# Kernel optimization log

Hardware: AMD Instinct MI355X
Metric: run time of the kernel (lower is better)

## Reference

```python
import jax, jax.numpy as jnp
import numpy as np

N, IN, OUT = 4096, 256, 256


def setup_inputs() -> dict:
    key = jax.random.key(0)
    k = jax.random.split(key, 7)
    return {
        "x": jax.random.normal(k[0], (N, IN), dtype=jnp.float32),
        "eps_w": jax.random.normal(k[1], (N, IN, OUT), dtype=jnp.float32),
        "eps_b": jax.random.normal(k[2], (N, OUT), dtype=jnp.float32),
        # learned parameters (init ranges per the torch module)
        "w_param1": jax.random.uniform(k[3], (IN, OUT), minval=-0.01, maxval=0.01, dtype=jnp.float32),
        "logw_param2": jax.random.uniform(k[4], (IN, OUT), minval=-4.0, maxval=-2.0, dtype=jnp.float32),
        "b_param1": jax.random.uniform(k[5], (OUT,), minval=-0.01, maxval=0.01, dtype=jnp.float32),
        "logb_param2": jax.random.uniform(k[6], (OUT,), minval=-4.0, maxval=-2.0, dtype=jnp.float32),
    }


def reference(x, eps_w, eps_b, w_param1, logw_param2, b_param1, logb_param2):
    # Per-sample reparameterized Gaussian weights: Normal(mu, exp(log_sigma)).sample((N,))
    weights = w_param1[None] + jnp.exp(logw_param2)[None] * eps_w   # [N, IN, OUT]
    biases = b_param1[None] + jnp.exp(logb_param2)[None] * eps_b    # [N, OUT]
    # (x.unsqueeze(1) @ weights).squeeze(1) + biases  ->  batched matvec
    return jnp.einsum("ni,nio->no", x, weights) + biases
```

## Files before the change

kernel.cpp:

```cpp
#include <hip/hip_runtime.h>

#define N_ROWS  4096
#define IN_DIM  256
#define OUT_DIM 256

#define RA 4
#define TA 256

#define RB 8
#define TB 512
#define TI 32
#define NTILES (IN_DIM / TI)

typedef float f32x4 __attribute__((ext_vector_type(4)));

__device__ __forceinline__ float4 nt_load4(const float4* p) {
    f32x4 v = __builtin_nontemporal_load((const f32x4*)p);
    return make_float4(v.x, v.y, v.z, v.w);
}

__global__ void bayes_exp_kernel(const float* __restrict__ logw,
                                 const float* __restrict__ logb,
                                 float* __restrict__ sw,
                                 float* __restrict__ sb) {
    int idx = blockIdx.x * blockDim.x + threadIdx.x;
    if (idx < IN_DIM * OUT_DIM) sw[idx] = __expf(logw[idx]);
    if (idx < OUT_DIM)          sb[idx] = __expf(logb[idx]);
}

template <bool PRE>
__global__ __launch_bounds__(TA) void bayes_base_kernel(
    const float* __restrict__ x,
    const float* __restrict__ eps_b,
    const float* __restrict__ w1,
    const float* __restrict__ b1,
    const float* __restrict__ sbl,
    float* __restrict__ out)
{
    __shared__ float xs[RA * IN_DIM];
    const int tid = threadIdx.x;
    const int n0  = blockIdx.x * RA;

    ((float4*)xs)[tid] = ((const float4*)(x + (size_t)n0 * IN_DIM))[tid];
    __syncthreads();

    const int row = tid >> 6;
    const int o4  = tid & 63;
    const int n   = n0 + row;

    const float4* w4 = (const float4*)w1 + o4;
    float4 acc = make_float4(0.f, 0.f, 0.f, 0.f);

    #pragma unroll 4
    for (int i = 0; i < IN_DIM; ++i) {
        const float  xv = xs[row * IN_DIM + i];
        const float4 w  = w4[i * (OUT_DIM / 4)];
        acc.x = fmaf(xv, w.x, acc.x);
        acc.y = fmaf(xv, w.y, acc.y);
        acc.z = fmaf(xv, w.z, acc.z);
        acc.w = fmaf(xv, w.w, acc.w);
    }

    const float4 eb = nt_load4((const float4*)(eps_b + (size_t)n * OUT_DIM) + o4);
    const float4 b  = ((const float4*)b1)[o4];
    float4 sb       = ((const float4*)sbl)[o4];
    if (!PRE) {
        sb.x = __expf(sb.x); sb.y = __expf(sb.y);
        sb.z = __expf(sb.z); sb.w = __expf(sb.w);
    }

    float4 res;
    res.x = acc.x + fmaf(sb.x, eb.x, b.x);
    res.y = acc.y + fmaf(sb.y, eb.y, b.y);
    res.z = acc.z + fmaf(sb.z, eb.z, b.z);
    res.w = acc.w + fmaf(sb.w, eb.w, b.w);

    ((float4*)(out + (size_t)n * OUT_DIM))[o4] = res;
}

template <bool PRE>
__global__ __launch_bounds__(TB) void bayes_eps_kernel(
    const float* __restrict__ x,
    const float* __restrict__ eps_w,
    const float* __restrict__ swl,
    float* __restrict__ out)
{
    __shared__ float xs[RB * IN_DIM];
    __shared__ float st[2 * TI * OUT_DIM];

    const int tid = threadIdx.x;
    const int n0  = blockIdx.x * RB;

    ((float4*)xs)[tid] = ((const float4*)(x + (size_t)n0 * IN_DIM))[tid];

    const int row = tid >> 6;
    const int o4  = tid & 63;
    const int n   = n0 + row;

    const float4* e4base = (const float4*)(eps_w + (size_t)n * IN_DIM * OUT_DIM) + o4;

    const float4 base = ((const float4*)(out + (size_t)n * OUT_DIM))[o4];

    #define STAGE(t, b)                                                        \
        do {                                                                   \
            const float4* _src = (const float4*)(swl + (t) * TI * OUT_DIM);    \
            float4 _v[4];                                                      \
            _Pragma("unroll")                                                  \
            for (int _k = 0; _k < 4; ++_k) _v[_k] = _src[tid + _k * TB];       \
            if (!PRE) {                                                        \
                _Pragma("unroll")                                              \
                for (int _k = 0; _k < 4; ++_k) {                               \
                    _v[_k].x = __expf(_v[_k].x); _v[_k].y = __expf(_v[_k].y);  \
                    _v[_k].z = __expf(_v[_k].z); _v[_k].w = __expf(_v[_k].w);  \
                }                                                              \
            }                                                                  \
            float4* _dst = (float4*)(st + (b) * TI * OUT_DIM);                 \
            _Pragma("unroll")                                                  \
            for (int _k = 0; _k < 4; ++_k) _dst[tid + _k * TB] = _v[_k];       \
        } while (0)

    STAGE(0, 0);

    float4 acc = make_float4(0.f, 0.f, 0.f, 0.f);
    int cur = 0;

    for (int t = 0; t < NTILES; ++t) {
        __syncthreads();
        if (t + 1 < NTILES) STAGE(t + 1, cur ^ 1);

        const float4* e4 = e4base + (size_t)t * TI * (OUT_DIM / 4);
        const float4* sp = (const float4*)(st + cur * TI * OUT_DIM);

        #pragma unroll 4
        for (int i = 0; i < TI; ++i) {
            const float  xv = xs[row * IN_DIM + t * TI + i];
            const float4 s  = sp[i * 64 + o4];
            const float4 e  = nt_load4(e4 + i * 64);
            acc.x = fmaf(xv * s.x, e.x, acc.x);
            acc.y = fmaf(xv * s.y, e.y, acc.y);
            acc.z = fmaf(xv * s.z, e.z, acc.z);
            acc.w = fmaf(xv * s.w, e.w, acc.w);
        }
        cur ^= 1;
    }
    #undef STAGE

    float4 res;
    res.x = base.x + acc.x;
    res.y = base.y + acc.y;
    res.z = base.z + acc.z;
    res.w = base.w + acc.w;
    ((float4*)(out + (size_t)n * OUT_DIM))[o4] = res;
}

extern "C" void kernel_launch(void* const* d_in, const int* in_sizes, int n_in,
                              void* d_out, int out_size, void* d_ws, size_t ws_size,
                              hipStream_t stream) {
    const float* x     = (const float*)d_in[0];
    const float* eps_w = (const float*)d_in[1];
    const float* eps_b = (const float*)d_in[2];
    const float* w1    = (const float*)d_in[3];
    const float* logw2 = (const float*)d_in[4];
    const float* b1    = (const float*)d_in[5];
    const float* logb2 = (const float*)d_in[6];
    float* out = (float*)d_out;

    const size_t need = (size_t)(IN_DIM * OUT_DIM + OUT_DIM) * sizeof(float);

    if (ws_size >= need) {
        float* sw = (float*)d_ws;
        float* sb = sw + IN_DIM * OUT_DIM;
        bayes_exp_kernel<<<(IN_DIM * OUT_DIM + 255) / 256, 256, 0, stream>>>(
            logw2, logb2, sw, sb);
        bayes_base_kernel<true><<<N_ROWS / RA, TA, 0, stream>>>(
            x, eps_b, w1, b1, sb, out);
        bayes_eps_kernel<true><<<N_ROWS / RB, TB, 0, stream>>>(
            x, eps_w, sw, out);
    } else {
        bayes_base_kernel<false><<<N_ROWS / RA, TA, 0, stream>>>(
            x, eps_b, w1, b1, logb2, out);
        bayes_eps_kernel<false><<<N_ROWS / RB, TB, 0, stream>>>(
            x, eps_w, logw2, out);
    }
}
```

Baseline: 209.1 us.

## Hold full bf16 sigma matrix in LDS and widen blocks to 1024 threads

The exponentiated sigma weights are now precomputed as bf16 and loaded whole into shared memory (128 KB) once per block. This replaces the double-buffered fp32 tile staging and its per-tile barriers. Blocks grow to 1024 threads covering 16 rows, and the bias exp moves into the base kernel so that kernel runs independently of the workspace. bf16 sigma loses precision, and the large LDS footprint allows only one block per CU, which may limit latency hiding for the eps_w stream that dominates the cost.

```diff
diff --git a/kernel.cpp b/kernel.cpp
--- a/kernel.cpp
+++ b/kernel.cpp
@@ -4,13 +4,10 @@
 #define IN_DIM  256
 #define OUT_DIM 256
 
-#define RA 4
-#define TA 256
-
-#define RB 8
-#define TB 512
-#define TI 32
-#define NTILES (IN_DIM / TI)
+#define TA 1024
+#define RA 16
+#define TB 1024
+#define RB 16
 
 typedef float f32x4 __attribute__((ext_vector_type(4)));
 
@@ -19,22 +16,27 @@
     return make_float4(v.x, v.y, v.z, v.w);
 }
 
-__global__ void bayes_exp_kernel(const float* __restrict__ logw,
-                                 const float* __restrict__ logb,
-                                 float* __restrict__ sw,
-                                 float* __restrict__ sb) {
-    int idx = blockIdx.x * blockDim.x + threadIdx.x;
-    if (idx < IN_DIM * OUT_DIM) sw[idx] = __expf(logw[idx]);
-    if (idx < OUT_DIM)          sb[idx] = __expf(logb[idx]);
+__device__ __forceinline__ unsigned short f32_to_bf16(float f) {
+    unsigned u = __float_as_uint(f);
+    u += 0x7FFFu + ((u >> 16) & 1u);
+    return (unsigned short)(u >> 16);
+}
+__device__ __forceinline__ float bf16_to_f32(unsigned short h) {
+    return __uint_as_float(((unsigned)h) << 16);
 }
 
-template <bool PRE>
+__global__ void bayes_exp_kernel(const float* __restrict__ logw,
+                                 unsigned short* __restrict__ swb) {
+    int idx = blockIdx.x * blockDim.x + threadIdx.x;
+    if (idx < IN_DIM * OUT_DIM) swb[idx] = f32_to_bf16(__expf(logw[idx]));
+}
+
 __global__ __launch_bounds__(TA) void bayes_base_kernel(
     const float* __restrict__ x,
     const float* __restrict__ eps_b,
     const float* __restrict__ w1,
     const float* __restrict__ b1,
-    const float* __restrict__ sbl,
+    const float* __restrict__ logb2,
     float* __restrict__ out)
 {
     __shared__ float xs[RA * IN_DIM];
@@ -63,17 +65,13 @@
 
     const float4 eb = nt_load4((const float4*)(eps_b + (size_t)n * OUT_DIM) + o4);
     const float4 b  = ((const float4*)b1)[o4];
-    float4 sb       = ((const float4*)sbl)[o4];
-    if (!PRE) {
-        sb.x = __expf(sb.x); sb.y = __expf(sb.y);
-        sb.z = __expf(sb.z); sb.w = __expf(sb.w);
-    }
+    const float4 lb = ((const float4*)logb2)[o4];
 
     float4 res;
-    res.x = acc.x + fmaf(sb.x, eb.x, b.x);
-    res.y = acc.y + fmaf(sb.y, eb.y, b.y);
-    res.z = acc.z + fmaf(sb.z, eb.z, b.z);
-    res.w = acc.w + fmaf(sb.w, eb.w, b.w);
+    res.x = acc.x + fmaf(__expf(lb.x), eb.x, b.x);
+    res.y = acc.y + fmaf(__expf(lb.y), eb.y, b.y);
+    res.z = acc.z + fmaf(__expf(lb.z), eb.z, b.z);
+    res.w = acc.w + fmaf(__expf(lb.w), eb.w, b.w);
 
     ((float4*)(out + (size_t)n * OUT_DIM))[o4] = res;
 }
@@ -82,75 +80,65 @@
 __global__ __launch_bounds__(TB) void bayes_eps_kernel(
     const float* __restrict__ x,
     const float* __restrict__ eps_w,
-    const float* __restrict__ swl,
+    const void*  __restrict__ swsrc,
     float* __restrict__ out)
 {
+    __shared__ uint4 swbuf[IN_DIM * OUT_DIM / 8];
     __shared__ float xs[RB * IN_DIM];
-    __shared__ float st[2 * TI * OUT_DIM];
 
     const int tid = threadIdx.x;
     const int n0  = blockIdx.x * RB;
 
+    if (PRE) {
+        const uint4* src = (const uint4*)swsrc;
+        #pragma unroll
+        for (int r = 0; r < 8; ++r)
+            swbuf[tid + r * TB] = src[tid + r * TB];
+    } else {
+        const float4* src = (const float4*)swsrc;
+        unsigned short* dst = (unsigned short*)swbuf;
+        #pragma unroll
+        for (int r = 0; r < 16; ++r) {
+            const int   j = tid + r * TB;
+            const float4 v = src[j];
+            ushort4 h;
+            h.x = f32_to_bf16(__expf(v.x));
+            h.y = f32_to_bf16(__expf(v.y));
+            h.z = f32_to_bf16(__expf(v.z));
+            h.w = f32_to_bf16(__expf(v.w));
+            *(ushort4*)(dst + j * 4) = h;
+        }
+    }
     ((float4*)xs)[tid] = ((const float4*)(x + (size_t)n0 * IN_DIM))[tid];
+    __syncthreads();
 
     const int row = tid >> 6;
     const int o4  = tid & 63;
     const int n   = n0 + row;
 
-    const float4* e4base = (const float4*)(eps_w + (size_t)n * IN_DIM * OUT_DIM) + o4;
-
-    const float4 base = ((const float4*)(out + (size_t)n * OUT_DIM))[o4];
-
-    #define STAGE(t, b)                                                        \
-        do {                                                                   \
-            const float4* _src = (const float4*)(swl + (t) * TI * OUT_DIM);    \
-            float4 _v[4];                                                      \
-            _Pragma("unroll")                                                  \
-            for (int _k = 0; _k < 4; ++_k) _v[_k] = _src[tid + _k * TB];       \
-            if (!PRE) {                                                        \
-                _Pragma("unroll")                                              \
-                for (int _k = 0; _k < 4; ++_k) {                               \
-                    _v[_k].x = __expf(_v[_k].x); _v[_k].y = __expf(_v[_k].y);  \
-                    _v[_k].z = __expf(_v[_k].z); _v[_k].w = __expf(_v[_k].w);  \
-                }                                                              \
-            }                                                                  \
-            float4* _dst = (float4*)(st + (b) * TI * OUT_DIM);                 \
-            _Pragma("unroll")                                                  \
-            for (int _k = 0; _k < 4; ++_k) _dst[tid + _k * TB] = _v[_k];       \
-        } while (0)
-
-    STAGE(0, 0);
+    const unsigned short* swp = (const unsigned short*)swbuf;
+    const float4* e4 = (const float4*)(eps_w + (size_t)n * IN_DIM * OUT_DIM) + o4;
 
     float4 acc = make_float4(0.f, 0.f, 0.f, 0.f);
-    int cur = 0;
 
-    for (int t = 0; t < NTILES; ++t) {
-        __syncthreads();
-        if (t + 1 < NTILES) STAGE(t + 1, cur ^ 1);
+    #pragma unroll 8
+    for (int i = 0; i < IN_DIM; ++i) {
+        const float   xv = xs[row * IN_DIM + i];
+        const ushort4 h  = *(const ushort4*)(swp + i * OUT_DIM + o4 * 4);
+        const float4  e  = nt_load4(e4 + i * (OUT_DIM / 4));
+        acc.x = fmaf(xv * bf16_to_f32(h.x), e.x, acc.x);
+        acc.y = fmaf(xv * bf16_to_f32(h.y), e.y, acc.y);
+        acc.z = fmaf(xv * bf16_to_f32(h.z), e.z, acc.z);
+        acc.w = fmaf(xv * bf16_to_f32(h.w), e.w, acc.w);
+    }
 
-        const float4* e4 = e4base + (size_t)t * TI * (OUT_DIM / 4);
-        const float4* sp = (const float4*)(st + cur * TI * OUT_DIM);
-
-        #pragma unroll 4
-        for (int i = 0; i < TI; ++i) {
-            const float  xv = xs[row * IN_DIM + t * TI + i];
-            const float4 s  = sp[i * 64 + o4];
-            const float4 e  = nt_load4(e4 + i * 64);
-            acc.x = fmaf(xv * s.x, e.x, acc.x);
-            acc.y = fmaf(xv * s.y, e.y, acc.y);
-            acc.z = fmaf(xv * s.z, e.z, acc.z);
-            acc.w = fmaf(xv * s.w, e.w, acc.w);
-        }
-        cur ^= 1;
-    }
-    #undef STAGE
-
-    float4 res;
-    res.x = base.x + acc.x;
-    res.y = base.y + acc.y;
-    res.z = base.z + acc.z;
-    res.w = base.w + acc.w;
-    ((float4*)(out + (size_t)n * OUT_DIM))[o4] = res;
+    float4* op = (float4*)(out + (size_t)n * OUT_DIM) + o4;
+    float4 base = *op;
+    base.x += acc.x;
+    base.y += acc.y;
+    base.z += acc.z;
+    base.w += acc.w;
+    *op = base;
 }
 
 extern "C" void kernel_launch(void* const* d_in, const int* in_sizes, int n_in,
@@ -165,20 +153,18 @@
     const float* logb2 = (const float*)d_in[6];
     float* out = (float*)d_out;
 
-    const size_t need = (size_t)(IN_DIM * OUT_DIM + OUT_DIM) * sizeof(float);
+    const size_t need = (size_t)(IN_DIM * OUT_DIM) * sizeof(unsigned short);
+
+    bayes_base_kernel<<<N_ROWS / RA, TA, 0, stream>>>(
+        x, eps_b, w1, b1, logb2, out);
 
     if (ws_size >= need) {
-        float* sw = (float*)d_ws;
-        float* sb = sw + IN_DIM * OUT_DIM;
-        bayes_exp_kernel<<<(IN_DIM * OUT_DIM + 255) / 256, 256, 0, stream>>>(
-            logw2, logb2, sw, sb);
-        bayes_base_kernel<true><<<N_ROWS / RA, TA, 0, stream>>>(
-            x, eps_b, w1, b1, sb, out);
+        unsigned short* swb = (unsigned short*)d_ws;
+        bayes_exp_kernel<<<(IN_DIM * OUT_DIM + 1023) / 1024, 1024, 0, stream>>>(
+            logw2, swb);
         bayes_eps_kernel<true><<<N_ROWS / RB, TB, 0, stream>>>(
-            x, eps_w, sw, out);
+            x, eps_w, swb, out);
     } else {
-        bayes_base_kernel<false><<<N_ROWS / RA, TA, 0, stream>>>(
-            x, eps_b, w1, b1, logb2, out);
         bayes_eps_kernel<false><<<N_ROWS / RB, TB, 0, stream>>>(
             x, eps_w, logw2, out);
     }
```

Result: no change. 210.9 us (+0.8%).
